# Performance work log

Hardware: AMD Instinct MI355X
Metric: run time of the kernel (lower is better)

## Reference

```python
import jax, jax.numpy as jnp
import numpy as np

EPS = 1e-5
CROSS = 12  # cross_size


def bn(x, g, b):
    # inference BatchNorm2d with running_mean=0, running_var=1
    s = g / jnp.sqrt(1.0 + EPS)
    return x * s[None, :, None, None] + b[None, :, None, None]


def conv1x1(x, w, b=None):
    # w: [out_c, in_c]
    y = jnp.einsum('bchw,oc->bohw', x, w)
    if b is not None:
        y = y + b[None, :, None, None]
    return y


def mlp(x, w1, b1, w2, b2):
    # Mlp with channels_first=True: 1x1 conv -> GELU -> 1x1 conv (drop=0)
    return conv1x1(jax.nn.gelu(conv1x1(x, w1, b1), approximate=False), w2, b2)


def setup_inputs() -> dict:
    key = jax.random.key(0)
    ks = jax.random.split(key, 24)
    B, Cl, Ch = 8, 128, 64
    Hl = Wl = 96
    Hh = Wh = 192

    def w(k, o, i):
        return jax.random.normal(k, (o, i), jnp.float32) / np.float32(np.sqrt(i))

    return {
        'x_l': jax.random.normal(ks[0], (B, Cl, Hl, Wl), jnp.float32),
        'x_h': jax.random.normal(ks[1], (B, Ch, Hh, Wh), jnp.float32),
        # mlp_l (hidden = in = Cl)
        'mlp_l_w1': w(ks[2], Cl, Cl), 'mlp_l_b1': jnp.zeros((Cl,), jnp.float32),
        'mlp_l_w2': w(ks[3], Cl, Cl), 'mlp_l_b2': jnp.zeros((Cl,), jnp.float32),
        # conv_1x1(Cl->Ch) + BN + ReLU
        'conv_w': w(ks[4], Ch, Cl),
        'conv_bn_g': jnp.ones((Ch,), jnp.float32), 'conv_bn_b': jnp.zeros((Ch,), jnp.float32),
        # cross_kv: BN(Cl) -> AdaptiveMaxPool(12,12) -> Conv1x1(Cl -> 2*Ch)
        'kv_bn_g': jnp.ones((Cl,), jnp.float32), 'kv_bn_b': jnp.zeros((Cl,), jnp.float32),
        'kv_w': w(ks[5], 2 * Ch, Cl), 'kv_b': jnp.zeros((2 * Ch,), jnp.float32),
        # self.norm: BN(Ch)
        'norm_g': jnp.ones((Ch,), jnp.float32), 'norm_b': jnp.zeros((Ch,), jnp.float32),
        # mlp_h
        'mlp_h_w1': w(ks[6], Ch, Ch), 'mlp_h_b1': jnp.zeros((Ch,), jnp.float32),
        'mlp_h_w2': w(ks[7], Ch, Ch), 'mlp_h_b2': jnp.zeros((Ch,), jnp.float32),
    }


def reference(x_l, x_h,
              mlp_l_w1, mlp_l_b1, mlp_l_w2, mlp_l_b2,
              conv_w, conv_bn_g, conv_bn_b,
              kv_bn_g, kv_bn_b, kv_w, kv_b,
              norm_g, norm_b,
              mlp_h_w1, mlp_h_b1, mlp_h_w2, mlp_h_b2):
    B, Cl, Hl, Wl = x_l.shape
    _, Ch, Hh, Wh = x_h.shape
    S = CROSS * CROSS  # 144

    # x_l = x_l + mlp_l(x_l)
    x_l = x_l + mlp(x_l, mlp_l_w1, mlp_l_b1, mlp_l_w2, mlp_l_b2)

    # x_h = x_h + interpolate(conv(x_l))
    x_l_conv = jax.nn.relu(bn(conv1x1(x_l, conv_w), conv_bn_g, conv_bn_b))
    up = jax.image.resize(x_l_conv, (B, Ch, Hh, Wh), method='linear')
    x_h = x_h + up

    # cross_kv(x_l): BN -> adaptive max pool to 12x12 -> 1x1 conv to 2*Ch
    xn_l = bn(x_l, kv_bn_g, kv_bn_b)
    pooled = xn_l.reshape(B, Cl, CROSS, Hl // CROSS, CROSS, Wl // CROSS).max(axis=(3, 5))
    kv = conv1x1(pooled, kv_w, kv_b)              # [B, 2*Ch, 12, 12]
    k, v = kv[:, :Ch], kv[:, Ch:]                 # each [B, Ch, 12, 12]
    k_mat = k.transpose(0, 2, 3, 1).reshape(B, S, Ch)  # grouped-conv kernel [B,S,Ch]
    v_mat = v.reshape(B, Ch, S)                        # grouped-conv kernel [B,Ch,S]

    # attn_h
    xn_h = bn(x_h, norm_g, norm_b)                # [B,Ch,Hh,Wh]
    attn = jnp.einsum('bchw,bsc->bshw', xn_h, k_mat)  # [B,S,Hh,Wh]
    attn = jax.nn.softmax(attn * (S ** -0.5), axis=1)
    out = jnp.einsum('bshw,bcs->bchw', attn, v_mat)   # [B,Ch,Hh,Wh]
    x_h = x_h + out

    # x_h = x_h + mlp_h(x_h)
    x_h = x_h + mlp(x_h, mlp_h_w1, mlp_h_b1, mlp_h_w2, mlp_h_b2)
    return x_h
```

## Files before the change

kernel.cpp:

```cpp
#include <hip/hip_runtime.h>
#include <math.h>

#define NB 8
#define CL 128
#define CH 64
#define HL 96
#define WL 96
#define PL (HL*WL)
#define HH 192
#define WH 192
#define PH (HH*WH)
#define NS 144
#define BN_S 0.9999950000374997f
#define INV12 (1.0f/12.0f)

typedef __attribute__((ext_vector_type(8))) short bf16x8;
typedef __attribute__((ext_vector_type(4))) float f32x4;
#define MFMA16(a,b,c) __builtin_amdgcn_mfma_f32_16x16x32_bf16(a,b,c,0,0,0)

__device__ __forceinline__ float gelu_exact(float x){
    return 0.5f*x*(1.0f + erff(x*0.7071067811865475f));
}
__device__ __forceinline__ short f2bf(float f){
    union { float f; unsigned u; } v; v.f = f;
    unsigned r = v.u + 0x7FFFu + ((v.u >> 16) & 1u);
    return (short)(r >> 16);
}

__global__ __launch_bounds__(256) void k_mlp_l(
    const float* __restrict__ xl, const float* __restrict__ w1, const float* __restrict__ b1,
    const float* __restrict__ w2, const float* __restrict__ b2, float* __restrict__ xl2)
{
    __shared__ short Wb[128*136];
    __shared__ short Xb[64*136];
    __shared__ float bS[256];
    const int tid = threadIdx.x;
    const int b   = blockIdx.x / (PL/64);
    const int hw0 = (blockIdx.x % (PL/64)) * 64;
    const float* xb = xl + (size_t)b*CL*PL + hw0;
    #pragma unroll
    for (int i=0;i<64;i++){ int idx=i*256+tid; Wb[(idx>>7)*136 + (idx&127)] = f2bf(w1[idx]); }
    #pragma unroll
    for (int i=0;i<32;i++){ int idx=i*256+tid; int c=idx>>6, p=idx&63;
        Xb[p*136+c] = f2bf(xb[(size_t)c*PL + p]); }
    if (tid < 128) bS[tid] = b1[tid]; else bS[tid] = b2[tid-128];
    __syncthreads();
    const int w = tid>>6, lane = tid&63, l16 = lane&15, q = lane>>4;
    const int pw = w*16;
    float hv[8][4];
    #pragma unroll
    for (int mt=0; mt<8; mt++){
        f32x4 acc = {0.f,0.f,0.f,0.f};
        #pragma unroll
        for (int k=0;k<4;k++){
            bf16x8 af = *(const bf16x8*)&Wb[(mt*16+l16)*136 + k*32 + q*8];
            bf16x8 bf = *(const bf16x8*)&Xb[(pw+l16)*136 + k*32 + q*8];
            acc = MFMA16(af, bf, acc);
        }
        #pragma unroll
        for (int r=0;r<4;r++) hv[mt][r] = gelu_exact(acc[r] + bS[mt*16+q*4+r]);
    }
    #pragma unroll
    for (int mt=0;mt<8;mt++)
        #pragma unroll
        for (int r=0;r<4;r++)
            Xb[(pw+l16)*136 + mt*16+q*4+r] = f2bf(hv[mt][r]);
    __syncthreads();
    #pragma unroll
    for (int i=0;i<64;i++){ int idx=i*256+tid; Wb[(idx>>7)*136 + (idx&127)] = f2bf(w2[idx]); }
    __syncthreads();
    float* yb = xl2 + (size_t)b*CL*PL + hw0;
    #pragma unroll
    for (int mt=0; mt<8; mt++){
        f32x4 acc = {0.f,0.f,0.f,0.f};
        #pragma unroll
        for (int k=0;k<4;k++){
            bf16x8 af = *(const bf16x8*)&Wb[(mt*16+l16)*136 + k*32 + q*8];
            bf16x8 bf = *(const bf16x8*)&Xb[(pw+l16)*136 + k*32 + q*8];
            acc = MFMA16(af, bf, acc);
        }
        #pragma unroll
        for (int r=0;r<4;r++){
            int o = mt*16 + q*4 + r;
            size_t off = (size_t)o*PL + pw + l16;
            yb[off] = acc[r] + bS[128+o] + xb[off];
        }
    }
}

__global__ __launch_bounds__(256) void k_conv_l(
    const float* __restrict__ xl2, const float* __restrict__ cw,
    const float* __restrict__ bng, const float* __restrict__ bnb, float* __restrict__ xc)
{
    __shared__ short Wb[64*136];
    __shared__ short Xb[64*136];
    const int tid = threadIdx.x;
    const int b   = blockIdx.x / (PL/64);
    const int hw0 = (blockIdx.x % (PL/64)) * 64;
    const float* xb = xl2 + (size_t)b*CL*PL + hw0;
    #pragma unroll
    for (int i=0;i<32;i++){ int idx=i*256+tid; Wb[(idx>>7)*136 + (idx&127)] = f2bf(cw[idx]); }
    #pragma unroll
    for (int i=0;i<32;i++){ int idx=i*256+tid; int c=idx>>6, p=idx&63;
        Xb[p*136+c] = f2bf(xb[(size_t)c*PL + p]); }
    __syncthreads();
    const int w = tid>>6, lane = tid&63, l16 = lane&15, q = lane>>4;
    const int pw = w*16;
    float* yb = xc + (size_t)b*CH*PL + hw0;
    #pragma unroll
    for (int mt=0; mt<4; mt++){
        f32x4 acc = {0.f,0.f,0.f,0.f};
        #pragma unroll
        for (int k=0;k<4;k++){
            bf16x8 af = *(const bf16x8*)&Wb[(mt*16+l16)*136 + k*32 + q*8];
            bf16x8 bf = *(const bf16x8*)&Xb[(pw+l16)*136 + k*32 + q*8];
            acc = MFMA16(af, bf, acc);
        }
        #pragma unroll
        for (int r=0;r<4;r++){
            int o = mt*16 + q*4 + r;
            float sc = bng[o]*BN_S, bb = bnb[o];
            yb[(size_t)o*PL + pw + l16] = fmaxf(sc*acc[r] + bb, 0.f);
        }
    }
}

__global__ __launch_bounds__(192) void k_pool(
    const float* __restrict__ xl2, const float* __restrict__ g, const float* __restrict__ bta,
    float* __restrict__ pooled)
{
    const int plane = blockIdx.x;
    const int tid = threadIdx.x;
    if (tid >= NS) return;
    const int c = plane & (CL-1);
    const float sc = g[c]*BN_S;
    const float tc = bta[c];
    const int i = tid/12, j = tid%12;
    const float* base = xl2 + (size_t)plane*PL + (size_t)i*8*WL + j*8;
    float m = -3.4e38f;
    #pragma unroll
    for (int dy=0;dy<8;dy++){
        const float* rr = base + dy*WL;
        #pragma unroll
        for (int dx=0;dx<8;dx++) m = fmaxf(m, sc*rr[dx]+tc);
    }
    pooled[(size_t)plane*NS + tid] = m;
}

__global__ __launch_bounds__(256) void k_kv(
    const float* __restrict__ pooled, const float* __restrict__ kvw, const float* __restrict__ kvb,
    const float* __restrict__ ng, const float* __restrict__ nb,
    float* __restrict__ keg, float* __restrict__ vg, float* __restrict__ biasg)
{
    const int t = blockIdx.x*256 + threadIdx.x;
    const int s = t % NS;
    const int r = t / NS;
    const int o = r & 127;
    const int b = r >> 7;
    const float* P = pooled + (size_t)b*CL*NS + s;
    const float* W = kvw + (size_t)o*CL;
    float acc = kvb[o];
    #pragma unroll 4
    for (int c=0;c<CL;c++) acc = fmaf(W[c], P[(size_t)c*NS], acc);
    if (o < CH){
        keg[((size_t)b*NS+s)*CH + o] = acc * (ng[o]*(BN_S*INV12));
        atomicAdd(&biasg[b*NS+s], acc * (nb[o]*INV12));
    } else {
        vg[((size_t)b*NS+s)*CH + (o-CH)] = acc;
    }
}

__global__ __launch_bounds__(256) void k_attn(
    const float* __restrict__ xh, const float* __restrict__ xc,
    const float* __restrict__ keg, const float* __restrict__ vg,
    const float* __restrict__ biasg,
    const float* __restrict__ w1h, const float* __restrict__ b1h,
    const float* __restrict__ w2h, const float* __restrict__ b2h,
    float* __restrict__ out)
{
    __shared__ short KVb[64*168];
    __shared__ short Xb[64*72];
    __shared__ short Pt[64*168];
    __shared__ float bS[NS];
    __shared__ float bH[128];
    const int tid = threadIdx.x;
    const int b   = blockIdx.x / (PH/64);
    const int hw0 = (blockIdx.x % (PH/64)) * 64;
    const int y   = hw0 / WH;
    const int xst = hw0 % WH;
    const int   lyr = (y>>1) - ((y&1)^1);
    const float fy  = (y&1) ? 0.25f : 0.75f;
    const int   y0i = lyr<0?0:lyr;
    const int   y1i = (lyr+1>HL-1)?(HL-1):(lyr+1);

    const float* xb  = xh + (size_t)b*CH*PH + hw0;
    const float* xcb = xc + (size_t)b*CH*PL;
    const float* keb = keg + (size_t)b*NS*CH;

    const int w = tid>>6, lane = tid&63, l16 = lane&15, q = lane>>4;
    const int pw = w*16;
    const int px = pw + l16;

    #pragma unroll
    for (int i=0;i<36;i++){ int idx=i*256+tid; KVb[(idx>>6)*72 + (idx&63)] = f2bf(keb[idx]); }
    if (tid < NS) bS[tid] = biasg[b*NS+tid];
    if (tid < 64) bH[tid] = b1h[tid]; else if (tid < 128) bH[tid] = b2h[tid-64];
    #pragma unroll
    for (int i=0;i<4;i++){ int idx=i*256+tid; Pt[(idx>>4)*168 + 144 + (idx&15)] = 0; }

    const int xo  = xst + px;
    const int lx  = (xo>>1) - ((xo&1)^1);
    const float fx = (xo&1) ? 0.25f : 0.75f;
    const int x0i = lx<0?0:lx;
    const int x1i = (lx+1>WL-1)?(WL-1):(lx+1);
    float resid[16];
    #pragma unroll
    for (int mt=0; mt<4; mt++)
        #pragma unroll
        for (int r=0; r<4; r++){
            int ch = mt*16 + q*4 + r;
            const float* s = xcb + (size_t)ch*PL;
            float v00 = s[y0i*WL+x0i], v01 = s[y0i*WL+x1i];
            float v10 = s[y1i*WL+x0i], v11 = s[y1i*WL+x1i];
            float top = v00 + fx*(v01-v00);
            float bot = v10 + fx*(v11-v10);
            float up  = top + fy*(bot-top);
            float val = xb[(size_t)ch*PH + px] + up;
            resid[mt*4+r] = val;
            Xb[px*72+ch] = f2bf(val);
        }
    __syncthreads();

    float ev[9][4];
    float mloc = -3.4e38f;
    #pragma unroll
    for (int st=0; st<9; st++){
        f32x4 acc = {0.f,0.f,0.f,0.f};
        #pragma unroll
        for (int k=0;k<2;k++){
            bf16x8 af = *(const bf16x8*)&KVb[(st*16+l16)*72 + k*32 + q*8];
            bf16x8 bf = *(const bf16x8*)&Xb[(pw+l16)*72 + k*32 + q*8];
            acc = MFMA16(af, bf, acc);
        }
        #pragma unroll
        for (int r=0;r<4;r++){
            float v = acc[r] + bS[st*16+q*4+r];
            ev[st][r] = v; mloc = fmaxf(mloc, v);
        }
    }
    mloc = fmaxf(mloc, __shfl_xor(mloc,16));
    mloc = fmaxf(mloc, __shfl_xor(mloc,32));
    float sloc = 0.f;
    #pragma unroll
    for (int st=0;st<9;st++)
        #pragma unroll
        for (int r=0;r<4;r++){ float e = __expf(ev[st][r]-mloc); ev[st][r]=e; sloc+=e; }
    sloc += __shfl_xor(sloc,16);
    sloc += __shfl_xor(sloc,32);
    const float rs = 1.f/sloc;
    #pragma unroll
    for (int st=0;st<9;st++)
        #pragma unroll
        for (int r=0;r<4;r++)
            Pt[(pw+l16)*168 + st*16+q*4+r] = f2bf(ev[st][r]);
    __syncthreads();
    const float* vb = vg + (size_t)b*NS*CH;
    #pragma unroll
    for (int i=0;i<36;i++){ int idx=i*256+tid; int s=idx>>6, c=idx&63;
        KVb[c*168 + s] = f2bf(vb[idx]); }
    #pragma unroll
    for (int i=0;i<4;i++){ int idx=i*256+tid; KVb[(idx>>4)*168 + 144 + (idx&15)] = 0; }
    __syncthreads();

    #pragma unroll
    for (int mt=0; mt<4; mt++){
        f32x4 acc = {0.f,0.f,0.f,0.f};
        #pragma unroll
        for (int k=0;k<5;k++){
            bf16x8 af = *(const bf16x8*)&KVb[(mt*16+l16)*168 + k*32 + q*8];
            bf16x8 bf = *(const bf16x8*)&Pt[(pw+l16)*168 + k*32 + q*8];
            acc = MFMA16(af, bf, acc);
        }
        #pragma unroll
        for (int r=0;r<4;r++){
            float v = resid[mt*4+r] + acc[r]*rs;
            resid[mt*4+r] = v;
            Xb[px*72 + mt*16+q*4+r] = f2bf(v);
        }
    }
    __syncthreads();
    #pragma unroll
    for (int i=0;i<16;i++){ int idx=i*256+tid; Pt[(idx>>6)*168 + (idx&63)] = f2bf(w1h[idx]); }
    #pragma unroll
    for (int i=0;i<16;i++){ int idx=i*256+tid; Pt[(idx>>6)*168 + 72 + (idx&63)] = f2bf(w2h[idx]); }
    __syncthreads();

    float hv[4][4];
    #pragma unroll
    for (int mt=0; mt<4; mt++){
        f32x4 acc = {0.f,0.f,0.f,0.f};
        #pragma unroll
        for (int k=0;k<2;k++){
            bf16x8 af = *(const bf16x8*)&Pt[(mt*16+l16)*168 + k*32 + q*8];
            bf16x8 bf = *(const bf16x8*)&Xb[(pw+l16)*72 + k*32 + q*8];
            acc = MFMA16(af, bf, acc);
        }
        #pragma unroll
        for (int r=0;r<4;r++) hv[mt][r] = gelu_exact(acc[r] + bH[mt*16+q*4+r]);
    }
    #pragma unroll
    for (int mt=0;mt<4;mt++)
        #pragma unroll
        for (int r=0;r<4;r++)
            Xb[px*72 + mt*16+q*4+r] = f2bf(hv[mt][r]);

    float* ob = out + (size_t)b*CH*PH + hw0;
    #pragma unroll
    for (int mt=0; mt<4; mt++){
        f32x4 acc = {0.f,0.f,0.f,0.f};
        #pragma unroll
        for (int k=0;k<2;k++){
            bf16x8 af = *(const bf16x8*)&Pt[(mt*16+l16)*168 + 72 + k*32 + q*8];
            bf16x8 bf = *(const bf16x8*)&Xb[(pw+l16)*72 + k*32 + q*8];
            acc = MFMA16(af, bf, acc);
        }
        #pragma unroll
        for (int r=0;r<4;r++){
            int ch = mt*16 + q*4 + r;
            ob[(size_t)ch*PH + px] = acc[r] + bH[64+ch] + resid[mt*4+r];
        }
    }
}

extern "C" void kernel_launch(void* const* d_in, const int* in_sizes, int n_in,
                              void* d_out, int out_size, void* d_ws, size_t ws_size,
                              hipStream_t stream)
{
    const float* xl    = (const float*)d_in[0];
    const float* xh    = (const float*)d_in[1];
    const float* ml_w1 = (const float*)d_in[2];
    const float* ml_b1 = (const float*)d_in[3];
    const float* ml_w2 = (const float*)d_in[4];
    const float* ml_b2 = (const float*)d_in[5];
    const float* cw    = (const float*)d_in[6];
    const float* cbg   = (const float*)d_in[7];
    const float* cbb   = (const float*)d_in[8];
    const float* kbg   = (const float*)d_in[9];
    const float* kbb   = (const float*)d_in[10];
    const float* kvw   = (const float*)d_in[11];
    const float* kvb   = (const float*)d_in[12];
    const float* ng    = (const float*)d_in[13];
    const float* nb    = (const float*)d_in[14];
    const float* mh_w1 = (const float*)d_in[15];
    const float* mh_b1 = (const float*)d_in[16];
    const float* mh_w2 = (const float*)d_in[17];
    const float* mh_b2 = (const float*)d_in[18];
    float* out = (float*)d_out;

    float* ws     = (float*)d_ws;
    float* xl2    = ws;
    float* xc     = xl2    + (size_t)NB*CL*PL;
    float* pooled = xc     + (size_t)NB*CH*PL;
    float* keg    = pooled + (size_t)NB*CL*NS;
    float* vg     = keg    + (size_t)NB*NS*CH;
    float* biasg  = vg     + (size_t)NB*NS*CH;

    k_mlp_l<<<dim3(NB*PL/64), dim3(256), 0, stream>>>(xl, ml_w1, ml_b1, ml_w2, ml_b2, xl2);
    k_conv_l<<<dim3(NB*PL/64), dim3(256), 0, stream>>>(xl2, cw, cbg, cbb, xc);
    k_pool<<<dim3(NB*CL), dim3(192), 0, stream>>>(xl2, kbg, kbb, pooled);
    hipMemsetAsync(biasg, 0, (size_t)NB*NS*sizeof(float), stream);
    k_kv<<<dim3((NB*128*NS)/256), dim3(256), 0, stream>>>(pooled, kvw, kvb, ng, nb, keg, vg, biasg);
    k_attn<<<dim3(NB*PH/64), dim3(256), 0, stream>>>(xh, xc, keg, vg, biasg,
                                                     mh_w1, mh_b1, mh_w2, mh_b2, out);
}
```

Before: 337.4 us.

## Fuse conv_l into mlp_l and vectorize bf16 LDS staging with packed converts

Merges the Cl->Ch conv+BN+ReLU kernel into the mlp_l kernel so xl2 is not re-read from global memory and one launch is removed. All fp32->bf16 shared-memory staging now uses float4 loads and v_cvt_pk_bf16_f32 packed stores instead of scalar conversions. The V matrix is stored channel-major so the attention kernel can load it with vector reads instead of a scattered transpose. The rounding mode of the hardware convert may differ slightly from the software rounding it replaces.

```diff
diff --git a/kernel.cpp b/kernel.cpp
--- a/kernel.cpp
+++ b/kernel.cpp
@@ -16,6 +16,7 @@
 
 typedef __attribute__((ext_vector_type(8))) short bf16x8;
 typedef __attribute__((ext_vector_type(4))) float f32x4;
+typedef __attribute__((ext_vector_type(2))) unsigned int uu2;
 #define MFMA16(a,b,c) __builtin_amdgcn_mfma_f32_16x16x32_bf16(a,b,c,0,0,0)
 
 __device__ __forceinline__ float gelu_exact(float x){
@@ -26,27 +27,50 @@
     unsigned r = v.u + 0x7FFFu + ((v.u >> 16) & 1u);
     return (short)(r >> 16);
 }
+__device__ __forceinline__ void st4(short* p, float a, float b, float c, float d){
+    uu2 r;
+    asm("v_cvt_pk_bf16_f32 %0, %1, %2" : "=v"(r.x) : "v"(a), "v"(b));
+    asm("v_cvt_pk_bf16_f32 %0, %1, %2" : "=v"(r.y) : "v"(c), "v"(d));
+    *(uu2*)p = r;
+}
+__device__ __forceinline__ void st4v(short* p, float4 v){ st4(p, v.x, v.y, v.z, v.w); }
 
 __global__ __launch_bounds__(256) void k_mlp_l(
     const float* __restrict__ xl, const float* __restrict__ w1, const float* __restrict__ b1,
-    const float* __restrict__ w2, const float* __restrict__ b2, float* __restrict__ xl2)
+    const float* __restrict__ w2, const float* __restrict__ b2,
+    const float* __restrict__ cw, const float* __restrict__ bng, const float* __restrict__ bnb,
+    float* __restrict__ xl2, float* __restrict__ xc)
 {
     __shared__ short Wb[128*136];
     __shared__ short Xb[64*136];
     __shared__ float bS[256];
+    __shared__ float bC[128];
     const int tid = threadIdx.x;
     const int b   = blockIdx.x / (PL/64);
     const int hw0 = (blockIdx.x % (PL/64)) * 64;
     const float* xb = xl + (size_t)b*CL*PL + hw0;
     #pragma unroll
-    for (int i=0;i<64;i++){ int idx=i*256+tid; Wb[(idx>>7)*136 + (idx&127)] = f2bf(w1[idx]); }
-    #pragma unroll
-    for (int i=0;i<32;i++){ int idx=i*256+tid; int c=idx>>6, p=idx&63;
-        Xb[p*136+c] = f2bf(xb[(size_t)c*PL + p]); }
+    for (int i=0;i<16;i++){
+        int idx4 = i*256+tid;
+        int row = idx4>>5, c4 = (idx4&31)<<2;
+        st4v(&Wb[row*136 + c4], *(const float4*)&w1[(row<<7) + c4]);
+    }
+    {
+        const int p = tid&63, wv = tid>>6;
+        #pragma unroll
+        for (int i=0;i<8;i++){
+            int c0 = wv*4 + i*16;
+            float a0 = xb[(size_t)(c0+0)*PL + p];
+            float a1 = xb[(size_t)(c0+1)*PL + p];
+            float a2 = xb[(size_t)(c0+2)*PL + p];
+            float a3 = xb[(size_t)(c0+3)*PL + p];
+            st4(&Xb[p*136 + c0], a0,a1,a2,a3);
+        }
+    }
     if (tid < 128) bS[tid] = b1[tid]; else bS[tid] = b2[tid-128];
     __syncthreads();
     const int w = tid>>6, lane = tid&63, l16 = lane&15, q = lane>>4;
-    const int pw = w*16;
+    const int pw = w*16, px = pw + l16;
     float hv[8][4];
     #pragma unroll
     for (int mt=0; mt<8; mt++){
@@ -62,12 +86,14 @@
     }
     #pragma unroll
     for (int mt=0;mt<8;mt++)
-        #pragma unroll
-        for (int r=0;r<4;r++)
-            Xb[(pw+l16)*136 + mt*16+q*4+r] = f2bf(hv[mt][r]);
-    __syncthreads();
-    #pragma unroll
-    for (int i=0;i<64;i++){ int idx=i*256+tid; Wb[(idx>>7)*136 + (idx&127)] = f2bf(w2[idx]); }
+        st4(&Xb[px*136 + mt*16 + q*4], hv[mt][0],hv[mt][1],hv[mt][2],hv[mt][3]);
+    __syncthreads();
+    #pragma unroll
+    for (int i=0;i<16;i++){
+        int idx4 = i*256+tid;
+        int row = idx4>>5, c4 = (idx4&31)<<2;
+        st4v(&Wb[row*136 + c4], *(const float4*)&w2[(row<<7) + c4]);
+    }
     __syncthreads();
     float* yb = xl2 + (size_t)b*CL*PL + hw0;
     #pragma unroll
@@ -82,31 +108,25 @@
         #pragma unroll
         for (int r=0;r<4;r++){
             int o = mt*16 + q*4 + r;
-            size_t off = (size_t)o*PL + pw + l16;
-            yb[off] = acc[r] + bS[128+o] + xb[off];
-        }
-    }
-}
-
-__global__ __launch_bounds__(256) void k_conv_l(
-    const float* __restrict__ xl2, const float* __restrict__ cw,
-    const float* __restrict__ bng, const float* __restrict__ bnb, float* __restrict__ xc)
-{
-    __shared__ short Wb[64*136];
-    __shared__ short Xb[64*136];
-    const int tid = threadIdx.x;
-    const int b   = blockIdx.x / (PL/64);
-    const int hw0 = (blockIdx.x % (PL/64)) * 64;
-    const float* xb = xl2 + (size_t)b*CL*PL + hw0;
-    #pragma unroll
-    for (int i=0;i<32;i++){ int idx=i*256+tid; Wb[(idx>>7)*136 + (idx&127)] = f2bf(cw[idx]); }
-    #pragma unroll
-    for (int i=0;i<32;i++){ int idx=i*256+tid; int c=idx>>6, p=idx&63;
-        Xb[p*136+c] = f2bf(xb[(size_t)c*PL + p]); }
-    __syncthreads();
-    const int w = tid>>6, lane = tid&63, l16 = lane&15, q = lane>>4;
-    const int pw = w*16;
-    float* yb = xc + (size_t)b*CH*PL + hw0;
+            size_t off = (size_t)o*PL + px;
+            float yy = acc[r] + bS[128+o] + xb[off];
+            yb[off] = yy;
+            hv[mt][r] = yy;
+        }
+    }
+    #pragma unroll
+    for (int mt=0;mt<8;mt++)
+        st4(&Xb[px*136 + mt*16 + q*4], hv[mt][0],hv[mt][1],hv[mt][2],hv[mt][3]);
+    __syncthreads();
+    #pragma unroll
+    for (int i=0;i<8;i++){
+        int idx4 = i*256+tid;
+        int row = idx4>>5, c4 = (idx4&31)<<2;
+        st4v(&Wb[row*136 + c4], *(const float4*)&cw[(row<<7) + c4]);
+    }
+    if (tid < 64) bC[tid] = bng[tid]*BN_S; else if (tid < 128) bC[tid] = bnb[tid-64];
+    __syncthreads();
+    float* cb = xc + (size_t)b*CH*PL + hw0;
     #pragma unroll
     for (int mt=0; mt<4; mt++){
         f32x4 acc = {0.f,0.f,0.f,0.f};
@@ -119,8 +139,7 @@
         #pragma unroll
         for (int r=0;r<4;r++){
             int o = mt*16 + q*4 + r;
-            float sc = bng[o]*BN_S, bb = bnb[o];
-            yb[(size_t)o*PL + pw + l16] = fmaxf(sc*acc[r] + bb, 0.f);
+            cb[(size_t)o*PL + px] = fmaxf(bC[o]*acc[r] + bC[64+o], 0.f);
         }
     }
 }
@@ -166,7 +185,7 @@
         keg[((size_t)b*NS+s)*CH + o] = acc * (ng[o]*(BN_S*INV12));
         atomicAdd(&biasg[b*NS+s], acc * (nb[o]*INV12));
     } else {
-        vg[((size_t)b*NS+s)*CH + (o-CH)] = acc;
+        vg[((size_t)b*CH + (o-CH))*NS + s] = acc;
     }
 }
 
@@ -198,15 +217,18 @@
     const float* keb = keg + (size_t)b*NS*CH;
 
     const int w = tid>>6, lane = tid&63, l16 = lane&15, q = lane>>4;
-    const int pw = w*16;
-    const int px = pw + l16;
-
-    #pragma unroll
-    for (int i=0;i<36;i++){ int idx=i*256+tid; KVb[(idx>>6)*72 + (idx&63)] = f2bf(keb[idx]); }
+    const int pw = w*16, px = pw + l16;
+
+    #pragma unroll
+    for (int i=0;i<9;i++){
+        int idx4 = i*256+tid;
+        int s = idx4>>4, c4 = (idx4&15)<<2;
+        st4v(&KVb[s*72 + c4], *(const float4*)&keb[(s<<6) + c4]);
+    }
     if (tid < NS) bS[tid] = biasg[b*NS+tid];
     if (tid < 64) bH[tid] = b1h[tid]; else if (tid < 128) bH[tid] = b2h[tid-64];
-    #pragma unroll
-    for (int i=0;i<4;i++){ int idx=i*256+tid; Pt[(idx>>4)*168 + 144 + (idx&15)] = 0; }
+    { int row = tid>>2, o4 = (tid&3)<<2;
+      *(uu2*)&Pt[row*168 + 144 + o4] = (uu2){0u,0u}; }
 
     const int xo  = xst + px;
     const int lx  = (xo>>1) - ((xo&1)^1);
@@ -215,7 +237,7 @@
     const int x1i = (lx+1>WL-1)?(WL-1):(lx+1);
     float resid[16];
     #pragma unroll
-    for (int mt=0; mt<4; mt++)
+    for (int mt=0; mt<4; mt++){
         #pragma unroll
         for (int r=0; r<4; r++){
             int ch = mt*16 + q*4 + r;
@@ -225,10 +247,11 @@
             float top = v00 + fx*(v01-v00);
             float bot = v10 + fx*(v11-v10);
             float up  = top + fy*(bot-top);
-            float val = xb[(size_t)ch*PH + px] + up;
-            resid[mt*4+r] = val;
-            Xb[px*72+ch] = f2bf(val);
-        }
+            resid[mt*4+r] = xb[(size_t)ch*PH + px] + up;
+        }
+        st4(&Xb[px*72 + mt*16 + q*4],
+            resid[mt*4+0], resid[mt*4+1], resid[mt*4+2], resid[mt*4+3]);
+    }
     __syncthreads();
 
     float ev[9][4];
@@ -260,16 +283,17 @@
     const float rs = 1.f/sloc;
     #pragma unroll
     for (int st=0;st<9;st++)
-        #pragma unroll
-        for (int r=0;r<4;r++)
-            Pt[(pw+l16)*168 + st*16+q*4+r] = f2bf(ev[st][r]);
-    __syncthreads();
-    const float* vb = vg + (size_t)b*NS*CH;
-    #pragma unroll
-    for (int i=0;i<36;i++){ int idx=i*256+tid; int s=idx>>6, c=idx&63;
-        KVb[c*168 + s] = f2bf(vb[idx]); }
-    #pragma unroll
-    for (int i=0;i<4;i++){ int idx=i*256+tid; KVb[(idx>>4)*168 + 144 + (idx&15)] = 0; }
+        st4(&Pt[px*168 + st*16 + q*4], ev[st][0], ev[st][1], ev[st][2], ev[st][3]);
+    __syncthreads();
+    const float* vb = vg + (size_t)b*CH*NS;
+    #pragma unroll
+    for (int i=0;i<9;i++){
+        int idx4 = i*256+tid;
+        int c = idx4/36, s4 = (idx4 - c*36)<<2;
+        st4v(&KVb[c*168 + s4], *(const float4*)&vb[c*NS + s4]);
+    }
+    { int row = tid>>2, o4 = (tid&3)<<2;
+      *(uu2*)&KVb[row*168 + 144 + o4] = (uu2){0u,0u}; }
     __syncthreads();
 
     #pragma unroll
@@ -282,17 +306,24 @@
             acc = MFMA16(af, bf, acc);
         }
         #pragma unroll
-        for (int r=0;r<4;r++){
-            float v = resid[mt*4+r] + acc[r]*rs;
-            resid[mt*4+r] = v;
-            Xb[px*72 + mt*16+q*4+r] = f2bf(v);
-        }
-    }
-    __syncthreads();
-    #pragma unroll
-    for (int i=0;i<16;i++){ int idx=i*256+tid; Pt[(idx>>6)*168 + (idx&63)] = f2bf(w1h[idx]); }
-    #pragma unroll
-    for (int i=0;i<16;i++){ int idx=i*256+tid; Pt[(idx>>6)*168 + 72 + (idx&63)] = f2bf(w2h[idx]); }
+        for (int r=0;r<4;r++)
+            resid[mt*4+r] = resid[mt*4+r] + acc[r]*rs;
+        st4(&Xb[px*72 + mt*16 + q*4],
+            resid[mt*4+0], resid[mt*4+1], resid[mt*4+2], resid[mt*4+3]);
+    }
+    __syncthreads();
+    #pragma unroll
+    for (int i=0;i<4;i++){
+        int idx4 = i*256+tid;
+        int o = idx4>>4, c4 = (idx4&15)<<2;
+        st4v(&Pt[o*168 + c4], *(const float4*)&w1h[(o<<6) + c4]);
+    }
+    #pragma unroll
+    for (int i=0;i<4;i++){
+        int idx4 = i*256+tid;
+        int o = idx4>>4, c4 = (idx4&15)<<2;
+        st4v(&Pt[o*168 + 72 + c4], *(const float4*)&w2h[(o<<6) + c4]);
+    }
     __syncthreads();
 
     float hv[4][4];
@@ -310,9 +341,7 @@
     }
     #pragma unroll
     for (int mt=0;mt<4;mt++)
-        #pragma unroll
-        for (int r=0;r<4;r++)
-            Xb[px*72 + mt*16+q*4+r] = f2bf(hv[mt][r]);
+        st4(&Xb[px*72 + mt*16 + q*4], hv[mt][0], hv[mt][1], hv[mt][2], hv[mt][3]);
 
     float* ob = out + (size_t)b*CH*PH + hw0;
     #pragma unroll
@@ -365,8 +394,8 @@
     float* vg     = keg    + (size_t)NB*NS*CH;
     float* biasg  = vg     + (size_t)NB*NS*CH;
 
-    k_mlp_l<<<dim3(NB*PL/64), dim3(256), 0, stream>>>(xl, ml_w1, ml_b1, ml_w2, ml_b2, xl2);
-    k_conv_l<<<dim3(NB*PL/64), dim3(256), 0, stream>>>(xl2, cw, cbg, cbb, xc);
+    k_mlp_l<<<dim3(NB*PL/64), dim3(256), 0, stream>>>(xl, ml_w1, ml_b1, ml_w2, ml_b2,
+                                                      cw, cbg, cbb, xl2, xc);
     k_pool<<<dim3(NB*CL), dim3(192), 0, stream>>>(xl2, kbg, kbb, pooled);
     hipMemsetAsync(biasg, 0, (size_t)NB*NS*sizeof(float), stream);
     k_kv<<<dim3((NB*128*NS)/256), dim3(256), 0, stream>>>(pooled, kvw, kvb, ng, nb, keg, vg, biasg);
```

New measurement: 306.3 us. 1.1x faster.
